# Kernel optimization log

Hardware: AMD Instinct MI355X
Metric: run time of the kernel (lower is better)

Reference implementation:

```python
import math
import jax, jax.numpy as jnp
import numpy as np

B, S, E, H = 2, 2048, 1024, 16
D = E // H  # head_dim = 64
NEG = jnp.float32(-1e9)  # finite stand-in for masked_fill(-inf) to avoid NaN in attn @ V


def setup_inputs() -> dict:
    key = jax.random.key(0)
    ks = jax.random.split(key, 8)
    inp = {
        "query": jax.random.normal(ks[0], (B, S, E), jnp.float32),
        "key": jax.random.normal(ks[1], (B, S, E), jnp.float32),
        "value": jax.random.normal(ks[2], (B, S, E), jnp.float32),
        "Wq": jax.random.normal(ks[3], (E, E), jnp.float32) * 0.02,
        "bq": jnp.zeros((E,), jnp.float32),
        "Wk": jax.random.normal(ks[4], (E, E), jnp.float32) * 0.02,
        "bk": jnp.zeros((E,), jnp.float32),
        "Wv": jax.random.normal(ks[5], (E, E), jnp.float32) * 0.02,
        "bv": jnp.zeros((E,), jnp.float32),
        "pos_bias": jax.random.normal(ks[6], (H, 2 * S - 1), jnp.float32) * 0.02,
    }
    # gather indices: per-head row index [H,1,1] and relative-position index [S,S]
    inp["idx0"] = jnp.arange(H, dtype=jnp.int32).reshape(H, 1, 1)
    rel = np.arange(S)[:, None] - np.arange(S)[None, :] + (S - 1)  # in [0, 2S-2]
    inp["idx1"] = jnp.asarray(rel, jnp.int32)
    # causal boolean mask: True where masked (j > i)
    inp["mask"] = jnp.triu(jnp.ones((S, S), jnp.bool_), k=1)
    return inp


def _split(x):  # [B,S,E] -> [B,H,S,D]
    return x.reshape(B, S, H, D).transpose(0, 2, 1, 3)


def reference(query, key, value, Wq, bq, Wk, bk, Wv, bv, pos_bias, idx0, idx1, mask):
    q = _split(query @ Wq.T + bq)
    k = _split(key @ Wk.T + bk)
    v = _split(value @ Wv.T + bv)
    logits = jnp.einsum("bhqd,bhkd->bhqk", q, k) / math.sqrt(D)  # [B,H,S,S]
    logits = logits + pos_bias[idx0, idx1]  # gather -> [H,S,S], broadcast over B
    logits = jnp.where(mask, NEG, logits)   # masked_fill
    attn = jax.nn.log_softmax(logits, axis=-1)  # module uses LogSoftmax (faithful)
    out = jnp.einsum("bhqk,bhkd->bhqd", attn, v)
    return out.transpose(0, 2, 1, 3).reshape(B, S, E)
```

## Files before the change

kernel.cpp:

```cpp
#include <hip/hip_runtime.h>
#include <math.h>

constexpr int BB = 2;
constexpr int SS = 2048;
constexpr int EE = 1024;
constexpr int HH = 16;
constexpr int DD = 64;

typedef short short8 __attribute__((ext_vector_type(8)));
typedef short short4_t __attribute__((ext_vector_type(4)));
typedef float floatx4 __attribute__((ext_vector_type(4)));
typedef unsigned short ushort_t;

__device__ __forceinline__ ushort_t f2bf(float f) {
    unsigned int u = __float_as_uint(f);
    u += 0x7fffu + ((u >> 16) & 1u);
    return (ushort_t)(u >> 16);
}
__device__ __forceinline__ float bf2f(short s) {
    return __uint_as_float(((unsigned)(ushort_t)s) << 16);
}

__device__ __forceinline__ void gl_lds16(const void* g, void* l) {
    __builtin_amdgcn_global_load_lds(
        (const __attribute__((address_space(1))) void*)g,
        (__attribute__((address_space(3))) void*)l, 16, 0, 0);
}

__global__ __launch_bounds__(256) void repack_all(
    const float* __restrict__ x0, const float* __restrict__ x1, const float* __restrict__ x2,
    const float* __restrict__ w0, const float* __restrict__ w1, const float* __restrict__ w2,
    ushort_t* __restrict__ Xbf, ushort_t* __restrict__ Wbf)
{
    const int idx = blockIdx.x * 256 + threadIdx.x;
    const int row = idx >> 7;
    const int gir = idx & 127;
    const float* src;
    ushort_t* dst;
    int r;
    if (row < 3 * BB * SS) {
        const int z = row >> 12; r = row & (BB * SS - 1);
        src = (z == 0) ? x0 : (z == 1) ? x1 : x2;
        dst = Xbf + (size_t)z * BB * SS * EE;
    } else {
        const int rw = row - 3 * BB * SS;
        const int z = rw >> 10; r = rw & (EE - 1);
        src = (z == 0) ? w0 : (z == 1) ? w1 : w2;
        dst = Wbf + (size_t)z * EE * EE;
    }
    const int blk = gir >> 3, g = gir & 7;
    const int gp = g ^ (r & 7);
    const float* sp = src + (size_t)r * EE + gir * 8;
    float4 a = *(const float4*)sp;
    float4 b = *(const float4*)(sp + 4);
    short8 o;
    o[0] = (short)f2bf(a.x); o[1] = (short)f2bf(a.y); o[2] = (short)f2bf(a.z); o[3] = (short)f2bf(a.w);
    o[4] = (short)f2bf(b.x); o[5] = (short)f2bf(b.y); o[6] = (short)f2bf(b.z); o[7] = (short)f2bf(b.w);
    *(short8*)&dst[(size_t)r * EE + blk * 64 + gp * 8] = o;
}

__global__ __launch_bounds__(256) void proj_kernel(
    const ushort_t* __restrict__ Xall, const ushort_t* __restrict__ Wall,
    const float* __restrict__ bq, const float* __restrict__ bk, const float* __restrict__ bv,
    ushort_t* __restrict__ qb, ushort_t* __restrict__ kbb, ushort_t* __restrict__ vtb)
{
    __shared__ __align__(16) ushort_t Xs[128 * 64];
    __shared__ __align__(16) ushort_t Ws[128 * 64];

    const int z = blockIdx.z;
    const ushort_t* X = Xall + (size_t)z * BB * SS * EE;
    const ushort_t* W = Wall + (size_t)z * EE * EE;
    const float* bias = (z == 0) ? bq : (z == 1) ? bk : bv;

    const int t = threadIdx.x, w = t >> 6, l = t & 63, ln = t & 15, qd = (t >> 4) & 3;
    const int row0 = blockIdx.x * 128;
    const int col0 = blockIdx.y * 128;
    const int wzm = (w & 1) * 64, wzn = (w >> 1) * 64;

    floatx4 acc[4][4];
    #pragma unroll
    for (int i = 0; i < 4; ++i)
        #pragma unroll
        for (int j = 0; j < 4; ++j)
            acc[i][j] = (floatx4){0.f, 0.f, 0.f, 0.f};

    for (int k0 = 0; k0 < EE; k0 += 64) {
        __syncthreads();
        #pragma unroll
        for (int j = 0; j < 4; ++j) {
            const int c = w * 4 + j;
            const int r = c * 8 + (l >> 3);
            gl_lds16(&X[(size_t)(row0 + r) * EE + k0 + (l & 7) * 8], &Xs[c * 512]);
            gl_lds16(&W[(size_t)(col0 + r) * EE + k0 + (l & 7) * 8], &Ws[c * 512]);
        }
        __syncthreads();

        const ushort_t* Am = (z < 2) ? Ws : Xs;
        const ushort_t* Bn = (z < 2) ? Xs : Ws;
        #pragma unroll
        for (int kh = 0; kh < 2; ++kh) {
            const int sw = ((kh * 4 + qd) ^ (ln & 7)) * 8;
            short8 af[4], bfr[4];
            #pragma unroll
            for (int mi = 0; mi < 4; ++mi)
                af[mi] = *(const short8*)&Am[(wzm + mi * 16 + ln) * 64 + sw];
            #pragma unroll
            for (int ni = 0; ni < 4; ++ni)
                bfr[ni] = *(const short8*)&Bn[(wzn + ni * 16 + ln) * 64 + sw];
            #pragma unroll
            for (int mi = 0; mi < 4; ++mi)
                #pragma unroll
                for (int ni = 0; ni < 4; ++ni)
                    acc[mi][ni] = __builtin_amdgcn_mfma_f32_16x16x32_bf16(af[mi], bfr[ni], acc[mi][ni], 0, 0, 0);
        }
    }

    if (z < 2) {
        ushort_t* dst = z ? kbb : qb;
        #pragma unroll
        for (int mi = 0; mi < 4; ++mi) {
            const int o0 = col0 + wzm + mi * 16 + qd * 4;
            const float4 b4 = *(const float4*)&bias[o0];
            const int h = o0 >> 6, d0 = o0 & 63;
            const int g = d0 >> 3, dlow = d0 & 7;
            #pragma unroll
            for (int ni = 0; ni < 4; ++ni) {
                const int s = row0 + wzn + ni * 16 + ln;
                const int b = s >> 11, sr = s & (SS - 1);
                const int gp = g ^ (sr & 7);
                short4_t pk;
                pk[0] = (short)f2bf(acc[mi][ni][0] + b4.x);
                pk[1] = (short)f2bf(acc[mi][ni][1] + b4.y);
                pk[2] = (short)f2bf(acc[mi][ni][2] + b4.z);
                pk[3] = (short)f2bf(acc[mi][ni][3] + b4.w);
                *(short4_t*)&dst[((size_t)((b * HH + h) * SS) + sr) * DD + gp * 8 + dlow] = pk;
            }
        }
    } else {
        #pragma unroll
        for (int mi = 0; mi < 4; ++mi) {
            const int s0 = row0 + wzm + mi * 16 + qd * 4;
            const int b = s0 >> 11, sr0 = s0 & (SS - 1);
            const int sg = (sr0 >> 3) & 7, slow = sr0 & 7;
            #pragma unroll
            for (int ni = 0; ni < 4; ++ni) {
                const int o = col0 + wzn + ni * 16 + ln;
                const int h = o >> 6, d = o & 63;
                const float bvv = bias[o];
                const int gp2 = sg ^ (d & 7);
                short4_t pk;
                pk[0] = (short)f2bf(acc[mi][ni][0] + bvv);
                pk[1] = (short)f2bf(acc[mi][ni][1] + bvv);
                pk[2] = (short)f2bf(acc[mi][ni][2] + bvv);
                pk[3] = (short)f2bf(acc[mi][ni][3] + bvv);
                *(short4_t*)&vtb[((size_t)((b * HH + h) * DD) + d) * SS + (sr0 & ~63) + gp2 * 8 + slow] = pk;
            }
        }
    }
}

__global__ __launch_bounds__(256) void scan_chunks(
    const ushort_t* __restrict__ vtb, float* __restrict__ segsuf)
{
    const int t = threadIdx.x;
    const int d = blockIdx.x * 8 + (t >> 5);
    const int ch = t & 31;
    const int bh = blockIdx.y;
    const ushort_t* src = vtb + ((size_t)(bh * DD + d)) * SS + ch * 64;
    float s = 0.f;
    #pragma unroll
    for (int i = 0; i < 8; ++i) {
        short8 v = *(const short8*)&src[i * 8];
        #pragma unroll
        for (int j = 0; j < 8; ++j) s += bf2f(v[j]);
    }
    #pragma unroll
    for (int delta = 1; delta < 32; delta <<= 1) {
        const float v = __shfl_down(s, delta, 32);
        if (ch + delta < 32) s += v;
    }
    segsuf[((size_t)bh * 33 + ch) * 64 + d] = s;
    if (ch == 31) segsuf[((size_t)bh * 33 + 32) * 64 + d] = 0.f;
}

__global__ __launch_bounds__(512, 4) void attn_kernel(
    const ushort_t* __restrict__ qb, const ushort_t* __restrict__ kbb,
    const ushort_t* __restrict__ vtb, const float* __restrict__ segsuf,
    const float* __restrict__ pb, float* __restrict__ out)
{
    __shared__ __align__(16) ushort_t Ks[2][64 * 64];
    __shared__ __align__(16) ushort_t Vt[2][64 * 64];
    __shared__ float pbL[2048];

    const int t = threadIdx.x, w = t >> 6, ln = t & 15, qd = (t >> 4) & 3;
    const int id = blockIdx.x, bh = id & 31, tt = id >> 5;
    const int qt = (tt < 8) ? (15 - tt) : (tt - 8);
    const int b = bh >> 4, h = bh & 15, i0 = qt * 128;
    const int r0 = 16 * w;

    {
        const float* p = pb + h * (2 * SS - 1) + (SS - 1);
        #pragma unroll
        for (int j = 0; j < 4; ++j) pbL[t * 4 + j] = p[t * 4 + j];
    }

    short8 qf[2];
    #pragma unroll
    for (int kh = 0; kh < 2; ++kh)
        qf[kh] = *(const short8*)&qb[((size_t)bh * SS + i0 + r0 + ln) * DD + (((kh * 4 + qd) ^ (ln & 7)) * 8)];

    floatx4 accpv[4], accsv[4];
    #pragma unroll
    for (int ct = 0; ct < 4; ++ct) {
        accpv[ct] = (floatx4){0.f, 0.f, 0.f, 0.f};
        accsv[ct] = (floatx4){0.f, 0.f, 0.f, 0.f};
    }
    float psum = 0.f;

    const int nkt = 2 * qt + 2;
    const int ownkt = 2 * qt + (w >> 2);
    const int iloc = (w & 3) * 16 + ln;

    auto stage = [&](int buf, int kt) {
        const int k0 = kt * 64;
        const int row = t >> 3, cg = t & 7;
        gl_lds16(&kbb[((size_t)bh * SS + k0 + row) * DD + cg * 8], &Ks[buf][w * 512]);
        gl_lds16(&vtb[((size_t)bh * DD + row) * SS + k0 + cg * 8], &Vt[buf][w * 512]);
    };

    stage(0, 0);
    for (int kt = 0; kt < nkt; ++kt) {
        __syncthreads();
        if (kt + 1 < nkt) stage((kt + 1) & 1, kt + 1);
        const int k0 = kt * 64, kdiag = i0 - k0;
        if (kdiag + r0 + 15 < 0) continue;
        const ushort_t* KsC = Ks[kt & 1];
        const ushort_t* VtC = Vt[kt & 1];

        floatx4 aq[4];
        #pragma unroll
        for (int mt = 0; mt < 4; ++mt) aq[mt] = (floatx4){0.f, 0.f, 0.f, 0.f};
        #pragma unroll
        for (int kh = 0; kh < 2; ++kh) {
            const int sw = ((kh * 4 + qd) ^ (ln & 7)) * 8;
            #pragma unroll
            for (int mt = 0; mt < 4; ++mt) {
                short8 af = *(const short8*)&KsC[(mt * 16 + ln) * 64 + sw];
                aq[mt] = __builtin_amdgcn_mfma_f32_16x16x32_bf16(af, qf[kh], aq[mt], 0, 0, 0);
            }
        }

        short4_t pfrag[4];
        const bool full = (kdiag + r0 >= 63);
        #pragma unroll
        for (int mt = 0; mt < 4; ++mt) {
            const int base = kdiag + r0 + ln - mt * 16 - qd * 4;
            #pragma unroll
            for (int reg = 0; reg < 4; ++reg) {
                if (full) {
                    const float val = aq[mt][reg] * 0.125f + pbL[base - reg];
                    psum += __expf(val);
                    pfrag[mt][reg] = (short)f2bf(val);
                } else {
                    const int rel = base - reg;
                    const bool ok = rel >= 0;
                    const float val = aq[mt][reg] * 0.125f + pbL[ok ? rel : 0];
                    psum += ok ? __expf(val) : 0.f;
                    pfrag[mt][reg] = ok ? (short)f2bf(val) : (short)0;
                }
            }
        }

        const bool own = (kt == ownkt);
        #pragma unroll
        for (int kk = 0; kk < 4; ++kk) {
            short4_t uf;
            if (own) {
                #pragma unroll
                for (int j = 0; j < 4; ++j)
                    uf[j] = (kk * 16 + qd * 4 + j > iloc) ? (short)0x3F80 : (short)0;
            }
            #pragma unroll
            for (int ct = 0; ct < 4; ++ct) {
                const int off = (ct * 16 + ln) * 64 + (((kk * 2 + (qd >> 1)) ^ (ln & 7)) * 8 + (qd & 1) * 4);
                short4_t bfr = *(const short4_t*)&VtC[off];
                accpv[ct] = __builtin_amdgcn_mfma_f32_16x16x16bf16_1k(pfrag[kk], bfr, accpv[ct], 0, 0, 0);
                if (own)
                    accsv[ct] = __builtin_amdgcn_mfma_f32_16x16x16bf16_1k(uf, bfr, accsv[ct], 0, 0, 0);
            }
        }
    }

    float p = psum;
    p += __shfl_xor(p, 16, 64);
    p += __shfl_xor(p, 32, 64);
    const float lseq = __logf(p);
    float lseR[4];
    #pragma unroll
    for (int reg = 0; reg < 4; ++reg)
        lseR[reg] = __shfl(lseq, qd * 4 + reg, 64);

    const int cmin = 2 * qt + (w >> 2) + 1;
    float tot[4], tail[4];
    #pragma unroll
    for (int ct = 0; ct < 4; ++ct) {
        const int d = ct * 16 + ln;
        tot[ct]  = segsuf[((size_t)bh * 33) * 64 + d];
        tail[ct] = segsuf[((size_t)bh * 33 + cmin) * 64 + d];
    }

    #pragma unroll
    for (int ct = 0; ct < 4; ++ct) {
        const int d = ct * 16 + ln;
        #pragma unroll
        for (int reg = 0; reg < 4; ++reg) {
            const int ig = i0 + r0 + qd * 4 + reg;
            const float o = accpv[ct][reg] - lseR[reg] * tot[ct]
                          - 1e9f * (accsv[ct][reg] + tail[ct]);
            out[((size_t)(b * SS + ig)) * EE + h * DD + d] = o;
        }
    }
}

extern "C" void kernel_launch(void* const* d_in, const int* in_sizes, int n_in,
                              void* d_out, int out_size, void* d_ws, size_t ws_size,
                              hipStream_t stream)
{
    const float* query = (const float*)d_in[0];
    const float* key_  = (const float*)d_in[1];
    const float* value = (const float*)d_in[2];
    const float* Wq = (const float*)d_in[3];
    const float* bq = (const float*)d_in[4];
    const float* Wk = (const float*)d_in[5];
    const float* bk = (const float*)d_in[6];
    const float* Wv = (const float*)d_in[7];
    const float* bv = (const float*)d_in[8];
    const float* pb = (const float*)d_in[9];
    float* out = (float*)d_out;

    float* ws = (float*)d_ws;
    const size_t SZ = (size_t)BB * SS * EE;
    float* segsuf = ws;
    ushort_t* us  = (ushort_t*)(segsuf + (size_t)BB * HH * 33 * DD);
    ushort_t* qbp = us;
    ushort_t* kbp = qbp + SZ;
    ushort_t* vtp = kbp + SZ;
    ushort_t* Xbf = vtp + SZ;
    ushort_t* Wbf = Xbf + 3 * SZ;

    const int ngroups = (3 * BB * SS + 3 * EE) * (EE / 8);
    repack_all<<<ngroups / 256, 256, 0, stream>>>(query, key_, value, Wq, Wk, Wv, Xbf, Wbf);

    proj_kernel<<<dim3(BB * SS / 128, EE / 128, 3), 256, 0, stream>>>(
        Xbf, Wbf, bq, bk, bv, qbp, kbp, vtp);

    scan_chunks<<<dim3(8, BB * HH), 256, 0, stream>>>(vtp, segsuf);

    attn_kernel<<<BB * HH * (SS / 128), 512, 0, stream>>>(
        qbp, kbp, vtp, segsuf, pb, out);
}
```

Measured before the change: 256.3 us.

## Shrink attention blocks to 64 queries and read K/V directly from global

The attention kernel now uses 256-thread blocks covering 64 query rows instead of 512 threads covering 128. It drops the LDS double-buffered K/V staging and its per-tile barriers, and has each wave load K and V fragments straight from global memory. The diagonal tile is peeled out of the main loop so full tiles skip the mask checks, and the exp-sum is split across two accumulators. This removes synchronisation and LDS traffic and doubles the number of blocks, at the cost of redundant global/L2 reads of K and V by every wave with no shared reuse.

```diff
diff --git a/kernel.cpp b/kernel.cpp
--- a/kernel.cpp
+++ b/kernel.cpp
@@ -183,26 +183,33 @@
     if (ch == 31) segsuf[((size_t)bh * 33 + 32) * 64 + d] = 0.f;
 }
 
-__global__ __launch_bounds__(512, 4) void attn_kernel(
+__global__ __launch_bounds__(256, 4) void attn_kernel(
     const ushort_t* __restrict__ qb, const ushort_t* __restrict__ kbb,
     const ushort_t* __restrict__ vtb, const float* __restrict__ segsuf,
     const float* __restrict__ pb, float* __restrict__ out)
 {
-    __shared__ __align__(16) ushort_t Ks[2][64 * 64];
-    __shared__ __align__(16) ushort_t Vt[2][64 * 64];
     __shared__ float pbL[2048];
 
     const int t = threadIdx.x, w = t >> 6, ln = t & 15, qd = (t >> 4) & 3;
-    const int id = blockIdx.x, bh = id & 31, tt = id >> 5;
-    const int qt = (tt < 8) ? (15 - tt) : (tt - 8);
-    const int b = bh >> 4, h = bh & 15, i0 = qt * 128;
+
+    const int id = blockIdx.x;
+    const int r_ = id & 255, g_ = id >> 8;
+    const int bh = r_ & 31, tq = r_ >> 5;
+    const int qt = (g_ == 0) ? (31 - tq)
+                 : (g_ == 1) ? (23 - tq)
+                 : (g_ == 2) ? (8 + tq) : tq;
+    const int b = bh >> 4, h = bh & 15, i0 = qt * 64;
     const int r0 = 16 * w;
 
     {
         const float* p = pb + h * (2 * SS - 1) + (SS - 1);
         #pragma unroll
-        for (int j = 0; j < 4; ++j) pbL[t * 4 + j] = p[t * 4 + j];
-    }
+        for (int j = 0; j < 8; ++j) pbL[t * 8 + j] = p[t * 8 + j];
+    }
+    __syncthreads();
+
+    const ushort_t* Kbh = kbb + (size_t)bh * SS * DD;
+    const ushort_t* Vbh = vtb + (size_t)bh * DD * SS;
 
     short8 qf[2];
     #pragma unroll
@@ -215,27 +222,10 @@
         accpv[ct] = (floatx4){0.f, 0.f, 0.f, 0.f};
         accsv[ct] = (floatx4){0.f, 0.f, 0.f, 0.f};
     }
-    float psum = 0.f;
-
-    const int nkt = 2 * qt + 2;
-    const int ownkt = 2 * qt + (w >> 2);
-    const int iloc = (w & 3) * 16 + ln;
-
-    auto stage = [&](int buf, int kt) {
+    float psum0 = 0.f, psum1 = 0.f;
+
+    for (int kt = 0; kt < qt; ++kt) {
         const int k0 = kt * 64;
-        const int row = t >> 3, cg = t & 7;
-        gl_lds16(&kbb[((size_t)bh * SS + k0 + row) * DD + cg * 8], &Ks[buf][w * 512]);
-        gl_lds16(&vtb[((size_t)bh * DD + row) * SS + k0 + cg * 8], &Vt[buf][w * 512]);
-    };
-
-    stage(0, 0);
-    for (int kt = 0; kt < nkt; ++kt) {
-        __syncthreads();
-        if (kt + 1 < nkt) stage((kt + 1) & 1, kt + 1);
-        const int k0 = kt * 64, kdiag = i0 - k0;
-        if (kdiag + r0 + 15 < 0) continue;
-        const ushort_t* KsC = Ks[kt & 1];
-        const ushort_t* VtC = Vt[kt & 1];
 
         floatx4 aq[4];
         #pragma unroll
@@ -245,53 +235,85 @@
             const int sw = ((kh * 4 + qd) ^ (ln & 7)) * 8;
             #pragma unroll
             for (int mt = 0; mt < 4; ++mt) {
-                short8 af = *(const short8*)&KsC[(mt * 16 + ln) * 64 + sw];
+                short8 af = *(const short8*)&Kbh[(size_t)(k0 + mt * 16 + ln) * DD + sw];
                 aq[mt] = __builtin_amdgcn_mfma_f32_16x16x32_bf16(af, qf[kh], aq[mt], 0, 0, 0);
             }
         }
 
         short4_t pfrag[4];
-        const bool full = (kdiag + r0 >= 63);
+        const int base0 = i0 - k0 + r0 + ln;
         #pragma unroll
         for (int mt = 0; mt < 4; ++mt) {
-            const int base = kdiag + r0 + ln - mt * 16 - qd * 4;
+            const int base = base0 - mt * 16 - qd * 4;
             #pragma unroll
             for (int reg = 0; reg < 4; ++reg) {
-                if (full) {
-                    const float val = aq[mt][reg] * 0.125f + pbL[base - reg];
-                    psum += __expf(val);
-                    pfrag[mt][reg] = (short)f2bf(val);
-                } else {
-                    const int rel = base - reg;
-                    const bool ok = rel >= 0;
-                    const float val = aq[mt][reg] * 0.125f + pbL[ok ? rel : 0];
-                    psum += ok ? __expf(val) : 0.f;
-                    pfrag[mt][reg] = ok ? (short)f2bf(val) : (short)0;
-                }
-            }
-        }
-
-        const bool own = (kt == ownkt);
+                const float val = aq[mt][reg] * 0.125f + pbL[base - reg];
+                if (reg & 1) psum1 += __expf(val); else psum0 += __expf(val);
+                pfrag[mt][reg] = (short)f2bf(val);
+            }
+        }
+
+        #pragma unroll
+        for (int kk = 0; kk < 4; ++kk) {
+            #pragma unroll
+            for (int ct = 0; ct < 4; ++ct) {
+                const size_t off = (size_t)(ct * 16 + ln) * SS + k0
+                                 + ((((kk * 2 + (qd >> 1)) ^ (ln & 7)) * 8) + (qd & 1) * 4);
+                short4_t bfr = *(const short4_t*)&Vbh[off];
+                accpv[ct] = __builtin_amdgcn_mfma_f32_16x16x16bf16_1k(pfrag[kk], bfr, accpv[ct], 0, 0, 0);
+            }
+        }
+    }
+
+    {
+        const int k0 = qt * 64;
+        const int iloc = r0 + ln;
+
+        floatx4 aq[4];
+        #pragma unroll
+        for (int mt = 0; mt < 4; ++mt) aq[mt] = (floatx4){0.f, 0.f, 0.f, 0.f};
+        #pragma unroll
+        for (int kh = 0; kh < 2; ++kh) {
+            const int sw = ((kh * 4 + qd) ^ (ln & 7)) * 8;
+            #pragma unroll
+            for (int mt = 0; mt < 4; ++mt) {
+                short8 af = *(const short8*)&Kbh[(size_t)(k0 + mt * 16 + ln) * DD + sw];
+                aq[mt] = __builtin_amdgcn_mfma_f32_16x16x32_bf16(af, qf[kh], aq[mt], 0, 0, 0);
+            }
+        }
+
+        short4_t pfrag[4];
+        #pragma unroll
+        for (int mt = 0; mt < 4; ++mt) {
+            const int base = r0 + ln - mt * 16 - qd * 4;
+            #pragma unroll
+            for (int reg = 0; reg < 4; ++reg) {
+                const int rel = base - reg;
+                const bool ok = rel >= 0;
+                const float val = aq[mt][reg] * 0.125f + pbL[ok ? rel : 0];
+                psum0 += ok ? __expf(val) : 0.f;
+                pfrag[mt][reg] = ok ? (short)f2bf(val) : (short)0;
+            }
+        }
+
         #pragma unroll
         for (int kk = 0; kk < 4; ++kk) {
             short4_t uf;
-            if (own) {
-                #pragma unroll
-                for (int j = 0; j < 4; ++j)
-                    uf[j] = (kk * 16 + qd * 4 + j > iloc) ? (short)0x3F80 : (short)0;
-            }
+            #pragma unroll
+            for (int j = 0; j < 4; ++j)
+                uf[j] = (kk * 16 + qd * 4 + j > iloc) ? (short)0x3F80 : (short)0;
             #pragma unroll
             for (int ct = 0; ct < 4; ++ct) {
-                const int off = (ct * 16 + ln) * 64 + (((kk * 2 + (qd >> 1)) ^ (ln & 7)) * 8 + (qd & 1) * 4);
-                short4_t bfr = *(const short4_t*)&VtC[off];
+                const size_t off = (size_t)(ct * 16 + ln) * SS + k0
+                                 + ((((kk * 2 + (qd >> 1)) ^ (ln & 7)) * 8) + (qd & 1) * 4);
+                short4_t bfr = *(const short4_t*)&Vbh[off];
                 accpv[ct] = __builtin_amdgcn_mfma_f32_16x16x16bf16_1k(pfrag[kk], bfr, accpv[ct], 0, 0, 0);
-                if (own)
-                    accsv[ct] = __builtin_amdgcn_mfma_f32_16x16x16bf16_1k(uf, bfr, accsv[ct], 0, 0, 0);
-            }
-        }
-    }
-
-    float p = psum;
+                accsv[ct] = __builtin_amdgcn_mfma_f32_16x16x16bf16_1k(uf, bfr, accsv[ct], 0, 0, 0);
+            }
+        }
+    }
+
+    float p = psum0 + psum1;
     p += __shfl_xor(p, 16, 64);
     p += __shfl_xor(p, 32, 64);
     const float lseq = __logf(p);
@@ -300,7 +322,7 @@
     for (int reg = 0; reg < 4; ++reg)
         lseR[reg] = __shfl(lseq, qd * 4 + reg, 64);
 
-    const int cmin = 2 * qt + (w >> 2) + 1;
+    const int cmin = qt + 1;
     float tot[4], tail[4];
     #pragma unroll
     for (int ct = 0; ct < 4; ++ct) {
@@ -356,6 +378,6 @@
 
     scan_chunks<<<dim3(8, BB * HH), 256, 0, stream>>>(vtp, segsuf);
 
-    attn_kernel<<<BB * HH * (SS / 128), 512, 0, stream>>>(
+    attn_kernel<<<BB * HH * (SS / 64), 256, 0, stream>>>(
         qbp, kbp, vtp, segsuf, pb, out);
 }
```

New measurement: 270.8 us. 1.06x slower.
